# Kernel optimization log

Hardware: AMD Instinct MI355X
Metric: run time of the kernel (lower is better)

## Reference

```python
import jax, jax.numpy as jnp
import numpy as np

# Problem sizes (match input_specs)
B, D, N, M, C = 2, 128, 131072, 131072, 128
IGNORE = -1  # config.data.ignore_label


def setup_inputs() -> dict:
    key = jax.random.key(0)
    k1, k2, k3, k4, k5 = jax.random.split(key, 5)
    vb = jax.random.randint(k1, (N, 1), 0, B)
    vxyz = jax.random.randint(k2, (N, 3), 0, D)
    coords = jnp.concatenate([vb, vxyz], axis=1).astype(jnp.int32)  # (N,4) [b,x,y,z]
    qb = jax.random.randint(k3, (M, 1), 0, B).astype(jnp.float32)
    qxyz = jax.random.uniform(k4, (M, 3), minval=0.0, maxval=float(D - 1))
    query_points = jnp.concatenate([qb, qxyz], axis=1)  # (M,4) [b,x,y,z]
    features = jax.random.normal(k5, (N, C), dtype=jnp.float32)  # (N,C)
    return {"coords": coords, "features": features, "query_points": query_points}


def reference(coords, features, query_points):
    n_vox = coords.shape[0]
    b = coords[:, 0]
    xyz = coords[:, 1:]
    # per-batch coordinate shift (torch.amin per batch), scale_factor == 1
    shift = jax.ops.segment_min(xyz, b, num_segments=B)  # (B,3)
    xyz = xyz - shift[b]
    qb = query_points[:, 0].astype(jnp.int32)
    q = query_points[:, 1:] - shift[qb].astype(query_points.dtype)  # (M,3)

    # dense occupancy: voxel index at occupied cells, IGNORE elsewhere
    occ = jnp.full((B, D, D, D), IGNORE, dtype=jnp.int32)
    occ = occ.at[b, xyz[:, 0], xyz[:, 1], xyz[:, 2]].set(
        jnp.arange(n_vox, dtype=jnp.int32))

    # 8-corner trilinear gather
    q0 = jnp.floor(q)
    f = q - q0                              # fractional part, (M,3)
    q0i = q0.astype(jnp.int32)
    offs = jnp.array([[i, j, k] for i in (0, 1) for j in (0, 1) for k in (0, 1)],
                     dtype=jnp.int32)       # (8,3)
    corner = q0i[:, None, :] + offs[None]   # (M,8,3)
    inb = jnp.all((corner >= 0) & (corner < D), axis=-1)  # (M,8)
    cc = jnp.clip(corner, 0, D - 1)
    idx = occ[qb[:, None], cc[..., 0], cc[..., 1], cc[..., 2]]  # (M,8)

    # trilinear weights: prod over dims of f (corner==1) or 1-f (corner==0)
    w = jnp.prod(jnp.where(offs[None].astype(bool), f[:, None, :], 1.0 - f[:, None, :]),
                 axis=-1)                   # (M,8)
    valid = inb & (idx >= 0)
    wv = jnp.where(valid, w, 0.0)
    wsum = wv.sum(-1)                       # (M,)

    safe_idx = jnp.clip(idx, 0, None)
    gathered = features[safe_idx]           # (M,8,C)
    query_features = jnp.einsum('mk,mkc->mc', wv, gathered) / \
        jnp.maximum(wsum, 1e-8)[:, None]    # normalized by valid weight mass

    interpolation_indices = jnp.where(valid, idx, IGNORE)
    accum_voxel_weights = jax.ops.segment_sum(
        wv.reshape(-1), safe_idx.reshape(-1), num_segments=n_vox)
    return query_features, interpolation_indices, wv, accum_voxel_weights
```

## Files before the change

### kernel.cpp

```cpp
#include <hip/hip_runtime.h>
#include <limits.h>

#define DIM 128
#define NVOX 131072
#define NQ 131072
#define NCELL (2 * DIM * DIM * DIM)
#define BITWORDS (NCELL / 64)

#define QF_OFF  0
#define IDX_OFF (NQ * 128)
#define WV_OFF  (IDX_OFF + NQ * 8)
#define ACC_OFF (WV_OFF + NQ * 8)

#define SHIFT_BLOCKS 64

typedef float vf2 __attribute__((ext_vector_type(2)));

#define WREDUCE_MIN(mv)                                       \
    _Pragma("unroll")                                         \
    for (int off = 32; off >= 1; off >>= 1)                   \
        mv = min(mv, __shfl_xor(mv, off, 64));

__device__ __forceinline__ int cell_of(int b, int x, int y, int z) {
    return (b << 21) + (x << 14) + (y << 7) + z;
}

__global__ __launch_bounds__(256) void k_prep(const int* __restrict__ coords,
                                              int* __restrict__ sp,
                                              unsigned long long* __restrict__ bitmap,
                                              int* __restrict__ idxg,
                                              float* __restrict__ accum) {
    int tid = blockIdx.x * 256 + threadIdx.x;
    int4 c = ((const int4*)coords)[tid];
    idxg[cell_of(c.x, c.y, c.z, c.w)] = -1;
    if (tid < BITWORDS) bitmap[tid] = 0ull;
    accum[tid] = 0.f;

    if (blockIdx.x < SHIFT_BLOCKS) {
        __shared__ int sm[4][6];
        int i0 = blockIdx.x * 256 + threadIdx.x;
        int sstride = SHIFT_BLOCKS * 256;
        int m0 = INT_MAX, m1 = INT_MAX, m2 = INT_MAX;
        int m3 = INT_MAX, m4 = INT_MAX, m5 = INT_MAX;
        const int4* c4 = (const int4*)coords;
        for (int i = i0; i < NVOX; i += sstride) {
            int4 v = c4[i];
            if (v.x == 0) { m0 = min(m0, v.y); m1 = min(m1, v.z); m2 = min(m2, v.w); }
            else          { m3 = min(m3, v.y); m4 = min(m4, v.z); m5 = min(m5, v.w); }
        }
        WREDUCE_MIN(m0) WREDUCE_MIN(m1) WREDUCE_MIN(m2)
        WREDUCE_MIN(m3) WREDUCE_MIN(m4) WREDUCE_MIN(m5)
        int wave = threadIdx.x >> 6;
        if ((threadIdx.x & 63) == 0) {
            sm[wave][0] = m0; sm[wave][1] = m1; sm[wave][2] = m2;
            sm[wave][3] = m3; sm[wave][4] = m4; sm[wave][5] = m5;
        }
        __syncthreads();
        if (threadIdx.x == 0) {
            #pragma unroll
            for (int k = 0; k < 6; ++k)
                sp[k * SHIFT_BLOCKS + blockIdx.x] =
                    min(min(sm[0][k], sm[1][k]), min(sm[2][k], sm[3][k]));
        }
    }
}

__global__ __launch_bounds__(256) void k_build(const int* __restrict__ coords,
                                               unsigned long long* __restrict__ bitmap,
                                               int* __restrict__ idxg) {
    int i = blockIdx.x * 256 + threadIdx.x;
    int4 c = ((const int4*)coords)[i];
    int cell = cell_of(c.x, c.y, c.z, c.w);
    atomicOr(&bitmap[cell >> 6], 1ull << (cell & 63));
    atomicMax(&idxg[cell], i);
}

__device__ __forceinline__ void load_shift(const int* __restrict__ sp, int* sh) {
    if (threadIdx.x < 64) {
        int l = threadIdx.x;
        #pragma unroll
        for (int k = 0; k < 6; ++k) {
            int v = sp[k * SHIFT_BLOCKS + l];
            WREDUCE_MIN(v)
            if (l == 0) sh[k] = v;
        }
    }
    __syncthreads();
}

__global__ __launch_bounds__(256) void k_query(
    const float* __restrict__ qpts, const float* __restrict__ feats,
    const unsigned long long* __restrict__ bitmap, const int* __restrict__ idxg,
    const int* __restrict__ sp, float* __restrict__ out) {
    __shared__ int sh[6];
    load_shift(sp, sh);

    int lane = threadIdx.x & 63;
    int gwave = blockIdx.x * 4 + (threadIdx.x >> 6);
    int qbase = gwave * 8;

    int qi = lane >> 3, k = lane & 7;
    int q = qbase + qi;
    float4 qp = ((const float4*)qpts)[q];
    int qb = (int)qp.x;
    float fx0 = floorf(qp.y), fy0 = floorf(qp.z), fz0 = floorf(qp.w);
    float fx = qp.y - fx0, fy = qp.z - fy0, fz = qp.w - fz0;
    int ox = (k >> 2) & 1, oy = (k >> 1) & 1, oz = k & 1;
    int ux = (int)fx0 + ox, uy = (int)fy0 + oy, uz = (int)fz0 + oz;
    bool inb = ((unsigned)(ux - sh[qb * 3 + 0]) < DIM) &&
               ((unsigned)(uy - sh[qb * 3 + 1]) < DIM) &&
               ((unsigned)(uz - sh[qb * 3 + 2]) < DIM);
    int cx = min(max(ux, 0), DIM - 1);
    int cy = min(max(uy, 0), DIM - 1);
    int cz = min(max(uz, 0), DIM - 1);
    int cell = cell_of(qb, cx, cy, cz);
    unsigned long long wbits = bitmap[cell >> 6];
    bool occb = ((wbits >> (cell & 63)) & 1ull) != 0ull
                && ((unsigned)ux < DIM) && ((unsigned)uy < DIM) && ((unsigned)uz < DIM);
    bool valid = inb && occb;
    int idx = 0;
    if (valid) idx = idxg[cell];

    float w = (ox ? fx : 1.f - fx) * (oy ? fy : 1.f - fy) * (oz ? fz : 1.f - fz);
    float wvk = valid ? w : 0.f;

    __builtin_nontemporal_store(valid ? (float)idx : -1.f,
                                out + IDX_OFF + (size_t)qbase * 8 + lane);
    __builtin_nontemporal_store(wvk, out + WV_OFF + (size_t)qbase * 8 + lane);
    if (valid && wvk != 0.f) atomicAdd(out + ACC_OFF + idx, wvk);

    float wsum = wvk;
    wsum += __shfl_xor(wsum, 1, 64);
    wsum += __shfl_xor(wsum, 2, 64);
    wsum += __shfl_xor(wsum, 4, 64);
    float inv = __builtin_amdgcn_rcpf(fmaxf(wsum, 1e-8f));

    int sidx = valid ? idx : 0;
    unsigned long long vm = __ballot(wvk != 0.f);
    const vf2* f2 = (const vf2*)feats;
    vf2 acc[8];
#pragma unroll
    for (int g = 0; g < 8; ++g) { acc[g] = (vf2){0.f, 0.f}; }
#pragma unroll
    for (int g = 0; g < 8; ++g) {
        unsigned int sub = (unsigned int)(vm >> (g * 8)) & 0xffu;
        while (sub) {
            int j = __ffs(sub) - 1; sub &= sub - 1;
            int src = g * 8 + j;
            float wv_j = __shfl(wvk, src, 64);
            int   idx_j = __shfl(sidx, src, 64);
            vf2 fv = f2[(size_t)idx_j * 64 + lane];
            acc[g].x = fmaf(wv_j, fv.x, acc[g].x);
            acc[g].y = fmaf(wv_j, fv.y, acc[g].y);
        }
    }

    vf2* qf = (vf2*)(out + QF_OFF);
#pragma unroll
    for (int g = 0; g < 8; ++g) {
        float iv = __shfl(inv, g * 8, 64);
        vf2 r;
        r.x = acc[g].x * iv;
        r.y = acc[g].y * iv;
        __builtin_nontemporal_store(r, qf + (size_t)(qbase + g) * 64 + lane);
    }
}

extern "C" void kernel_launch(void* const* d_in, const int* in_sizes, int n_in,
                              void* d_out, int out_size, void* d_ws, size_t ws_size,
                              hipStream_t stream) {
    const int*   coords = (const int*)d_in[0];
    const float* feats  = (const float*)d_in[1];
    const float* qpts   = (const float*)d_in[2];
    float* out = (float*)d_out;

    int* sp = (int*)d_ws;
    unsigned long long* bitmap = (unsigned long long*)((char*)d_ws + 4096);
    int* idxg = (int*)((char*)d_ws + 4096 + BITWORDS * 8);

    k_prep<<<NVOX / 256, 256, 0, stream>>>(coords, sp, bitmap, idxg, out + ACC_OFF);
    k_build<<<NVOX / 256, 256, 0, stream>>>(coords, bitmap, idxg);
    k_query<<<NQ / 32, 256, 0, stream>>>(qpts, feats, bitmap, idxg, sp, out);
}
```

Measured before the change: 46.32 us.

## Map one query per thread and stage corner indices through LDS for gather

The query kernel now gives each thread one query and all eight of its corners, instead of one corner per lane with eight queries per wave. Corner indices, weights and masks are staged in shared memory and then written out in coalesced order. The feature gather loops over 64 queries per wave, using readfirstlane to get uniform rows. This cuts the number of blocks and the shuffle traffic, but it adds LDS use (about 18KB per block), lowers occupancy, and serializes the gather loop over 64 queries per wave.

After: 45.53 us. No clear change (-1.7%).

```diff
diff --git a/kernel.cpp b/kernel.cpp
--- a/kernel.cpp
+++ b/kernel.cpp
@@ -85,7 +85,6 @@
             if (l == 0) sh[k] = v;
         }
     }
-    __syncthreads();
 }
 
 __global__ __launch_bounds__(256) void k_query(
@@ -93,76 +92,93 @@
     const unsigned long long* __restrict__ bitmap, const int* __restrict__ idxg,
     const int* __restrict__ sp, float* __restrict__ out) {
     __shared__ int sh[6];
+    __shared__ int2  s_iw[256 * 8];
+    __shared__ uint2 s_mi[256];
     load_shift(sp, sh);
-
-    int lane = threadIdx.x & 63;
-    int gwave = blockIdx.x * 4 + (threadIdx.x >> 6);
-    int qbase = gwave * 8;
-
-    int qi = lane >> 3, k = lane & 7;
-    int q = qbase + qi;
+    __syncthreads();
+
+    int t = threadIdx.x;
+    int q = blockIdx.x * 256 + t;
+
     float4 qp = ((const float4*)qpts)[q];
     int qb = (int)qp.x;
+    int shx = sh[qb * 3 + 0], shy = sh[qb * 3 + 1], shz = sh[qb * 3 + 2];
     float fx0 = floorf(qp.y), fy0 = floorf(qp.z), fz0 = floorf(qp.w);
     float fx = qp.y - fx0, fy = qp.z - fy0, fz = qp.w - fz0;
-    int ox = (k >> 2) & 1, oy = (k >> 1) & 1, oz = k & 1;
-    int ux = (int)fx0 + ox, uy = (int)fy0 + oy, uz = (int)fz0 + oz;
-    bool inb = ((unsigned)(ux - sh[qb * 3 + 0]) < DIM) &&
-               ((unsigned)(uy - sh[qb * 3 + 1]) < DIM) &&
-               ((unsigned)(uz - sh[qb * 3 + 2]) < DIM);
-    int cx = min(max(ux, 0), DIM - 1);
-    int cy = min(max(uy, 0), DIM - 1);
-    int cz = min(max(uz, 0), DIM - 1);
-    int cell = cell_of(qb, cx, cy, cz);
-    unsigned long long wbits = bitmap[cell >> 6];
-    bool occb = ((wbits >> (cell & 63)) & 1ull) != 0ull
-                && ((unsigned)ux < DIM) && ((unsigned)uy < DIM) && ((unsigned)uz < DIM);
-    bool valid = inb && occb;
-    int idx = 0;
-    if (valid) idx = idxg[cell];
-
-    float w = (ox ? fx : 1.f - fx) * (oy ? fy : 1.f - fy) * (oz ? fz : 1.f - fz);
-    float wvk = valid ? w : 0.f;
-
-    __builtin_nontemporal_store(valid ? (float)idx : -1.f,
-                                out + IDX_OFF + (size_t)qbase * 8 + lane);
-    __builtin_nontemporal_store(wvk, out + WV_OFF + (size_t)qbase * 8 + lane);
-    if (valid && wvk != 0.f) atomicAdd(out + ACC_OFF + idx, wvk);
-
-    float wsum = wvk;
-    wsum += __shfl_xor(wsum, 1, 64);
-    wsum += __shfl_xor(wsum, 2, 64);
-    wsum += __shfl_xor(wsum, 4, 64);
+    int ix = (int)fx0, iy = (int)fy0, iz = (int)fz0;
+
+    int cells[8]; bool okc[8]; float wc[8];
+#pragma unroll
+    for (int k = 0; k < 8; ++k) {
+        const int ox = (k >> 2) & 1, oy = (k >> 1) & 1, oz = k & 1;
+        int ux = ix + ox, uy = iy + oy, uz = iz + oz;
+        okc[k] = ((unsigned)(ux - shx) < DIM) && ((unsigned)(uy - shy) < DIM) &&
+                 ((unsigned)(uz - shz) < DIM) &&
+                 ((unsigned)ux < DIM) && ((unsigned)uy < DIM) && ((unsigned)uz < DIM);
+        int cx = min(max(ux, 0), DIM - 1);
+        int cy = min(max(uy, 0), DIM - 1);
+        int cz = min(max(uz, 0), DIM - 1);
+        cells[k] = cell_of(qb, cx, cy, cz);
+        wc[k] = (ox ? fx : 1.f - fx) * (oy ? fy : 1.f - fy) * (oz ? fz : 1.f - fz);
+    }
+    unsigned long long wb[8];
+#pragma unroll
+    for (int k = 0; k < 8; ++k) wb[k] = bitmap[cells[k] >> 6];
+    bool val[8];
+#pragma unroll
+    for (int k = 0; k < 8; ++k)
+        val[k] = okc[k] && (((wb[k] >> (cells[k] & 63)) & 1ull) != 0ull);
+    int idxk[8];
+#pragma unroll
+    for (int k = 0; k < 8; ++k) idxk[k] = val[k] ? idxg[cells[k]] : -1;
+
+    float wsum = 0.f; unsigned msk = 0u;
+#pragma unroll
+    for (int k = 0; k < 8; ++k) {
+        float wv = val[k] ? wc[k] : 0.f;
+        wsum += wv;
+        if (wv != 0.f) {
+            msk |= 1u << k;
+            atomicAdd(out + ACC_OFF + idxk[k], wv);
+        }
+        s_iw[t * 8 + k] = make_int2(idxk[k], __float_as_int(wv));
+    }
     float inv = __builtin_amdgcn_rcpf(fmaxf(wsum, 1e-8f));
-
-    int sidx = valid ? idx : 0;
-    unsigned long long vm = __ballot(wvk != 0.f);
+    s_mi[t] = make_uint2(msk, __float_as_uint(inv));
+    __syncthreads();
+
+    size_t sbase = (size_t)blockIdx.x * 2048;
+#pragma unroll
+    for (int j = 0; j < 8; ++j) {
+        int2 iw = s_iw[j * 256 + t];
+        __builtin_nontemporal_store((float)iw.x, out + IDX_OFF + sbase + j * 256 + t);
+        __builtin_nontemporal_store(__int_as_float(iw.y), out + WV_OFF + sbase + j * 256 + t);
+    }
+
+    int lane = t & 63;
+    int wq0 = (t >> 6) * 64;
     const vf2* f2 = (const vf2*)feats;
-    vf2 acc[8];
-#pragma unroll
-    for (int g = 0; g < 8; ++g) { acc[g] = (vf2){0.f, 0.f}; }
-#pragma unroll
-    for (int g = 0; g < 8; ++g) {
-        unsigned int sub = (unsigned int)(vm >> (g * 8)) & 0xffu;
-        while (sub) {
-            int j = __ffs(sub) - 1; sub &= sub - 1;
-            int src = g * 8 + j;
-            float wv_j = __shfl(wvk, src, 64);
-            int   idx_j = __shfl(sidx, src, 64);
-            vf2 fv = f2[(size_t)idx_j * 64 + lane];
-            acc[g].x = fmaf(wv_j, fv.x, acc[g].x);
-            acc[g].y = fmaf(wv_j, fv.y, acc[g].y);
-        }
-    }
-
     vf2* qf = (vf2*)(out + QF_OFF);
-#pragma unroll
-    for (int g = 0; g < 8; ++g) {
-        float iv = __shfl(inv, g * 8, 64);
+    size_t qgbase = (size_t)blockIdx.x * 256;
+    for (int g = 0; g < 64; ++g) {
+        int qq = wq0 + g;
+        uint2 mi = s_mi[qq];
+        unsigned m = __builtin_amdgcn_readfirstlane(mi.x);
+        vf2 acc = (vf2){0.f, 0.f};
+        while (m) {
+            int j = __ffs(m) - 1; m &= m - 1;
+            int2 iw = s_iw[qq * 8 + j];
+            int row = __builtin_amdgcn_readfirstlane(iw.x);
+            float wv = __int_as_float(iw.y);
+            vf2 fv = f2[(size_t)row * 64 + lane];
+            acc.x = fmaf(wv, fv.x, acc.x);
+            acc.y = fmaf(wv, fv.y, acc.y);
+        }
+        float iv = __uint_as_float(mi.y);
         vf2 r;
-        r.x = acc[g].x * iv;
-        r.y = acc[g].y * iv;
-        __builtin_nontemporal_store(r, qf + (size_t)(qbase + g) * 64 + lane);
+        r.x = acc.x * iv;
+        r.y = acc.y * iv;
+        __builtin_nontemporal_store(r, qf + (qgbase + qq) * 64 + lane);
     }
 }
 
@@ -180,5 +196,5 @@
 
     k_prep<<<NVOX / 256, 256, 0, stream>>>(coords, sp, bitmap, idxg, out + ACC_OFF);
     k_build<<<NVOX / 256, 256, 0, stream>>>(coords, bitmap, idxg);
-    k_query<<<NQ / 32, 256, 0, stream>>>(qpts, feats, bitmap, idxg, sp, out);
-}
+    k_query<<<NQ / 256, 256, 0, stream>>>(qpts, feats, bitmap, idxg, sp, out);
+}
```
